# Kernel optimization log

Hardware: AMD Instinct MI355X
Metric: run time of the kernel (lower is better)

Reference implementation:

```python
import jax, jax.numpy as jnp
import numpy as np

KH = KW = 3
STRIDE = 1
PAD = 0


def _unfold(x, kh, kw, stride, pad):
    # x: (N, C, H, W) -> (N, L, K) with K ordered (c, i, j) like torch.nn.functional.unfold
    N, C, H, W = x.shape
    if pad:
        x = jnp.pad(x, ((0, 0), (0, 0), (pad, pad), (pad, pad)))
        H, W = H + 2 * pad, W + 2 * pad
    Hout = (H - kh) // stride + 1
    Wout = (W - kw) // stride + 1
    patches = [
        x[:, :, i:i + stride * Hout:stride, j:j + stride * Wout:stride]
        for i in range(kh) for j in range(kw)
    ]
    p = jnp.stack(patches, axis=2)            # (N, C, kh*kw, Hout, Wout)
    p = p.reshape(N, C * kh * kw, Hout * Wout)  # (N, K, L), K = c*kh*kw + i*kw + j
    return jnp.transpose(p, (0, 2, 1)), Hout, Wout  # (N, L, K)


def setup_inputs() -> dict:
    key = jax.random.key(0)
    k1, k2, k3 = jax.random.split(key, 3)
    N, C, H, W = 64, 32, 64, 64
    O = 64
    L = (H - KH + 1) * (W - KW + 1)  # 3844
    K = KH * KW * C                  # 288
    x = jax.random.normal(k1, (N, C, H, W), dtype=jnp.float32)
    weight = jax.random.normal(k2, (O, L, K), dtype=jnp.float32)
    bias = jax.random.normal(k3, (O, L), dtype=jnp.float32)
    return {"x": x, "weight": weight, "bias": bias}


def reference(x, weight, bias):
    # Locally connected layer: per-spatial-location weights, no weight sharing.
    x_unf, Hout, Wout = _unfold(x, KH, KW, STRIDE, PAD)   # (N, L, K)
    out = jnp.einsum('nlk,olk->nol', x_unf, weight)        # (N, O, L)
    out = out + bias[None, :, :]
    N, O, L = out.shape
    return out.reshape(N, O, Hout, Wout)
```

## Files before the change

### kernel.cpp

```cpp
#include <hip/hip_runtime.h>


#define L_TOT 3844
#define K_TOT 288
#define LDS_STRIDE 68

__global__ __launch_bounds__(256, 4)
void lc_fp32_kernel(const float* __restrict__ x,
                    const float* __restrict__ w,
                    const float* __restrict__ b,
                    float* __restrict__ out) {
    __shared__ float Xs[32][LDS_STRIDE];
    __shared__ float Ws[32][LDS_STRIDE];
    __shared__ int offs[K_TOT];

    const int tid = threadIdx.x;

    for (int k = tid; k < K_TOT; k += 256) {
        int c = k / 9, rem = k % 9;
        offs[k] = c * 4096 + (rem / 3) * 64 + (rem % 3);
    }

    const int orig = blockIdx.x;
    const int xcd = orig & 7;
    const int slot = orig >> 3;
    const int l = (xcd < 4) ? (xcd * 481 + slot)
                            : (1924 + (xcd - 4) * 480 + slot);

    const int ho = l / 62, wo = l % 62;
    const int xbase = ho * 64 + wo;

    const int tx = tid & 15;
    const int ty = tid >> 4;

    float acc[4][4] = {{0.f}};

    __syncthreads();

    for (int kk = 0; kk < K_TOT; kk += 32) {
        #pragma unroll
        for (int p = 0; p < 8; ++p) {
            int idx = (p << 8) + tid;
            int n = idx >> 5, k = idx & 31;
            Xs[k][n] = x[n * 131072 + xbase + offs[kk + k]];
        }
        #pragma unroll
        for (int p = 0; p < 8; ++p) {
            int idx = (p << 8) + tid;
            int o = idx >> 5, k = idx & 31;
            Ws[k][o] = w[(o * L_TOT + l) * K_TOT + kk + k];
        }
        __syncthreads();

        #pragma unroll
        for (int k = 0; k < 32; ++k) {
            const float4 av = *(const float4*)(&Xs[k][ty * 4]);
            const float4 bv = *(const float4*)(&Ws[k][tx * 4]);
            const float am[4] = {av.x, av.y, av.z, av.w};
            const float bm[4] = {bv.x, bv.y, bv.z, bv.w};
            #pragma unroll
            for (int m = 0; m < 4; ++m)
                #pragma unroll
                for (int j = 0; j < 4; ++j)
                    acc[m][j] = fmaf(am[m], bm[j], acc[m][j]);
        }
        __syncthreads();
    }

    float bv[4];
    #pragma unroll
    for (int j = 0; j < 4; ++j) bv[j] = b[(tx * 4 + j) * L_TOT + l];

    #pragma unroll
    for (int m = 0; m < 4; ++m) {
        const int n = ty * 4 + m;
        #pragma unroll
        for (int j = 0; j < 4; ++j) {
            const int o = tx * 4 + j;
            out[(n * 64 + o) * L_TOT + l] = acc[m][j] + bv[j];
        }
    }
}

extern "C" void kernel_launch(void* const* d_in, const int* in_sizes, int n_in,
                              void* d_out, int out_size, void* d_ws, size_t ws_size,
                              hipStream_t stream) {
    const float* x = (const float*)d_in[0];
    const float* w = (const float*)d_in[1];
    const float* b = (const float*)d_in[2];
    float* out = (float*)d_out;

    hipLaunchKernelGGL(lc_fp32_kernel, dim3(L_TOT), dim3(256), 0, stream,
                       x, w, b, out);
}
```

Baseline: 602.0 us.

## Process four spatial locations per block with double-buffered LDS and 8x8 register tiles

Each block now handles four consecutive output locations (one per wavefront), so the grid shrinks by four. Each thread computes an 8x8 register tile over K chunks of 8, and the global loads for the next chunk are issued before the current chunk is computed, using ping-pong LDS buffers. The epilogue goes through LDS so bias adds and output stores are float4 writes across the four adjacent locations. The per-wave tiles are larger, which raises register pressure and may lower occupancy under the launch bound of 4 blocks per CU.

Result: slower. 805.6 us (+33.8%).

```diff
diff --git a/kernel.cpp b/kernel.cpp
--- a/kernel.cpp
+++ b/kernel.cpp
@@ -3,81 +3,158 @@
 
 #define L_TOT 3844
 #define K_TOT 288
-#define LDS_STRIDE 68
+#define KC 8
+#define NCH 36
+#define ROW 68
+#define TILE_F (4 * KC * ROW)
 
 __global__ __launch_bounds__(256, 4)
 void lc_fp32_kernel(const float* __restrict__ x,
-                    const float* __restrict__ w,
-                    const float* __restrict__ b,
+                    const float* __restrict__ wgt,
+                    const float* __restrict__ bias,
                     float* __restrict__ out) {
-    __shared__ float Xs[32][LDS_STRIDE];
-    __shared__ float Ws[32][LDS_STRIDE];
+    __shared__ __align__(16) float smem[4 * TILE_F];
     __shared__ int offs[K_TOT];
 
     const int tid = threadIdx.x;
 
     for (int k = tid; k < K_TOT; k += 256) {
-        int c = k / 9, rem = k % 9;
-        offs[k] = c * 4096 + (rem / 3) * 64 + (rem % 3);
+        int c = k / 9, r = k % 9;
+        offs[k] = c * 4096 + (r / 3) * 64 + (r % 3);
     }
 
     const int orig = blockIdx.x;
-    const int xcd = orig & 7;
-    const int slot = orig >> 3;
-    const int l = (xcd < 4) ? (xcd * 481 + slot)
-                            : (1924 + (xcd - 4) * 480 + slot);
+    const int xcd = orig & 7, slot = orig >> 3;
+    const int lg = (xcd == 0) ? slot : (121 + (xcd - 1) * 120 + slot);
+    const int lbase = lg * 4;
 
-    const int ho = l / 62, wo = l % 62;
-    const int xbase = ho * 64 + wo;
+    const int kq = tid & 7;
+    const int t8 = tid >> 3;
+    const int ow  = (tid >> 1) & 63;
+    const int th  = tid >> 7;
+    const int k4w = tid & 1;
 
-    const int tx = tid & 15;
-    const int ty = tid >> 4;
+    int xb[4];
+#pragma unroll
+    for (int li = 0; li < 4; ++li) {
+        int l = lbase + li;
+        xb[li] = (l / 62) * 64 + (l % 62);
+    }
+    const float* xP = x + t8 * 131072;
+    const int wgb = ow * (L_TOT * K_TOT) + (lbase + th) * K_TOT + k4w * 4;
+    const int xw  = kq * ROW + t8;
+    const int wwb = th * 544 + k4w * 272 + ow;
 
-    float acc[4][4] = {{0.f}};
+    const int wv = tid >> 6;
+    const int lane = tid & 63;
+    const int tx = lane & 7;
+    const int ty = lane >> 3;
+
+    float* Xb0 = smem;
+    float* Wb0 = smem + TILE_F;
+    float* Xb1 = smem + 2 * TILE_F;
+    float* Wb1 = smem + 3 * TILE_F;
+
+    float acc[8][8];
+#pragma unroll
+    for (int m = 0; m < 8; ++m)
+#pragma unroll
+        for (int j = 0; j < 8; ++j) acc[m][j] = 0.f;
+
+    float xv[8];
+    float4 wv4[2];
+
+#define STAGE_LOAD(ch)                                                        \
+    {                                                                         \
+        const int kk = (ch) * KC;                                             \
+        const int offk = offs[kk + kq];                                       \
+        _Pragma("unroll")                                                     \
+        for (int e = 0; e < 8; ++e)                                           \
+            xv[e] = xP[(e & 1) * 4194304 + xb[e >> 1] + offk];                \
+        wv4[0] = *(const float4*)(wgt + wgb + kk);                            \
+        wv4[1] = *(const float4*)(wgt + wgb + 576 + kk);                      \
+    }
+
+#define STAGE_WRITE(XB, WB)                                                   \
+    {                                                                         \
+        _Pragma("unroll")                                                     \
+        for (int e = 0; e < 8; ++e)                                           \
+            XB[(e >> 1) * 544 + (e & 1) * 32 + xw] = xv[e];                   \
+        _Pragma("unroll")                                                     \
+        for (int e = 0; e < 2; ++e) {                                         \
+            WB[wwb + e * 1088]       = wv4[e].x;                              \
+            WB[wwb + e * 1088 + 68]  = wv4[e].y;                              \
+            WB[wwb + e * 1088 + 136] = wv4[e].z;                              \
+            WB[wwb + e * 1088 + 204] = wv4[e].w;                              \
+        }                                                                     \
+    }
+
+#define COMPUTE(XB, WB)                                                       \
+    {                                                                         \
+        _Pragma("unroll")                                                     \
+        for (int k = 0; k < KC; ++k) {                                        \
+            const float4 a0 = *(const float4*)(XB + wv*544 + k*68 + ty*8);    \
+            const float4 a1 = *(const float4*)(XB + wv*544 + k*68 + ty*8 + 4);\
+            const float4 b0 = *(const float4*)(WB + wv*544 + k*68 + tx*8);    \
+            const float4 b1 = *(const float4*)(WB + wv*544 + k*68 + tx*8 + 4);\
+            const float av[8] = {a0.x,a0.y,a0.z,a0.w,a1.x,a1.y,a1.z,a1.w};    \
+            const float bw[8] = {b0.x,b0.y,b0.z,b0.w,b1.x,b1.y,b1.z,b1.w};    \
+            _Pragma("unroll")                                                 \
+            for (int m = 0; m < 8; ++m)                                       \
+                _Pragma("unroll")                                             \
+                for (int j = 0; j < 8; ++j)                                   \
+                    acc[m][j] = fmaf(av[m], bw[j], acc[m][j]);                \
+        }                                                                     \
+    }
 
     __syncthreads();
+    STAGE_LOAD(0);
+    STAGE_WRITE(Xb0, Wb0);
+    __syncthreads();
 
-    for (int kk = 0; kk < K_TOT; kk += 32) {
-        #pragma unroll
-        for (int p = 0; p < 8; ++p) {
-            int idx = (p << 8) + tid;
-            int n = idx >> 5, k = idx & 31;
-            Xs[k][n] = x[n * 131072 + xbase + offs[kk + k]];
-        }
-        #pragma unroll
-        for (int p = 0; p < 8; ++p) {
-            int idx = (p << 8) + tid;
-            int o = idx >> 5, k = idx & 31;
-            Ws[k][o] = w[(o * L_TOT + l) * K_TOT + kk + k];
-        }
+    for (int ch = 0; ch < NCH; ch += 2) {
+        STAGE_LOAD(ch + 1);
+        COMPUTE(Xb0, Wb0);
+        STAGE_WRITE(Xb1, Wb1);
         __syncthreads();
-
-        #pragma unroll
-        for (int k = 0; k < 32; ++k) {
-            const float4 av = *(const float4*)(&Xs[k][ty * 4]);
-            const float4 bv = *(const float4*)(&Ws[k][tx * 4]);
-            const float am[4] = {av.x, av.y, av.z, av.w};
-            const float bm[4] = {bv.x, bv.y, bv.z, bv.w};
-            #pragma unroll
-            for (int m = 0; m < 4; ++m)
-                #pragma unroll
-                for (int j = 0; j < 4; ++j)
-                    acc[m][j] = fmaf(am[m], bm[j], acc[m][j]);
+        if (ch + 2 < NCH) {
+            STAGE_LOAD(ch + 2);
+            COMPUTE(Xb1, Wb1);
+            STAGE_WRITE(Xb0, Wb0);
+        } else {
+            COMPUTE(Xb1, Wb1);
         }
         __syncthreads();
     }
 
-    float bv[4];
-    #pragma unroll
-    for (int j = 0; j < 4; ++j) bv[j] = b[(tx * 4 + j) * L_TOT + l];
+    float* Es = smem;
+    const int h_owner = ty >> 2;
+    const int typ = ty & 3;
+    const float4 bv4 = *(const float4*)(bias + lane * L_TOT + lbase);
 
-    #pragma unroll
-    for (int m = 0; m < 4; ++m) {
-        const int n = ty * 4 + m;
-        #pragma unroll
-        for (int j = 0; j < 4; ++j) {
-            const int o = tx * 4 + j;
-            out[(n * 64 + o) * L_TOT + l] = acc[m][j] + bv[j];
+#pragma unroll
+    for (int h = 0; h < 2; ++h) {
+        if (h == 1) __syncthreads();
+        if (h_owner == h) {
+#pragma unroll
+            for (int m = 0; m < 8; ++m) {
+                *(float4*)(Es + wv*2176 + (typ*8 + m)*68 + tx*8) =
+                    make_float4(acc[m][0], acc[m][1], acc[m][2], acc[m][3]);
+                *(float4*)(Es + wv*2176 + (typ*8 + m)*68 + tx*8 + 4) =
+                    make_float4(acc[m][4], acc[m][5], acc[m][6], acc[m][7]);
+            }
+        }
+        __syncthreads();
+#pragma unroll
+        for (int e = 0; e < 8; ++e) {
+            const int np = e * 4 + wv;
+            float4 sv;
+            sv.x = Es[           np*68 + lane];
+            sv.y = Es[1*2176 +   np*68 + lane];
+            sv.z = Es[2*2176 +   np*68 + lane];
+            sv.w = Es[3*2176 +   np*68 + lane];
+            sv.x += bv4.x; sv.y += bv4.y; sv.z += bv4.z; sv.w += bv4.w;
+            *(float4*)(out + ((h*32 + np)*64 + lane) * L_TOT + lbase) = sv;
         }
     }
 }
@@ -90,6 +167,6 @@
     const float* b = (const float*)d_in[2];
     float* out = (float*)d_out;
 
-    hipLaunchKernelGGL(lc_fp32_kernel, dim3(L_TOT), dim3(256), 0, stream,
+    hipLaunchKernelGGL(lc_fp32_kernel, dim3(L_TOT / 4), dim3(256), 0, stream,
                        x, w, b, out);
 }
```
